# Kernel tuning notes

Hardware: AMD Instinct MI355X
Metric: run time of the kernel (lower is better)

## Reference

```python
import jax, jax.numpy as jnp
import numpy as np

B, K, L, D, H = 8, 64, 4096, 1024, 16
HD = D // H
SCALE = HD ** -0.5


def setup_inputs() -> dict:
    key = jax.random.key(0)
    ks = jax.random.split(key, 7)
    return {
        "query": jax.random.normal(ks[0], (B, K, D), jnp.float32),
        "key": jax.random.normal(ks[1], (B, L, D), jnp.float32),
        "value": jax.random.normal(ks[2], (B, L, D), jnp.float32),
        "Wq": jax.random.normal(ks[3], (D, D), jnp.float32) * (D ** -0.5),
        "Wk": jax.random.normal(ks[4], (D, D), jnp.float32) * (D ** -0.5),
        "Wv": jax.random.normal(ks[5], (D, D), jnp.float32) * (D ** -0.5),
        "Wo": jax.random.normal(ks[6], (D, D), jnp.float32) * (D ** -0.5),
        "bo": jnp.zeros((D,), jnp.float32),
    }


def reference(query, key, value, Wq, Wk, Wv, Wo, bo):
    # torch Linear: y = x @ W.T; split heads -> [B,H,len,HD]
    q = jnp.einsum('bkd,ed->bke', query, Wq).reshape(B, K, H, HD).transpose(0, 2, 1, 3)
    k = jnp.einsum('bld,ed->ble', key, Wk).reshape(B, L, H, HD).transpose(0, 2, 1, 3)
    v = jnp.einsum('bld,ed->ble', value, Wv).reshape(B, L, H, HD).transpose(0, 2, 1, 3)
    dots = jnp.einsum('bhkc,bhlc->bhkl', q, k) * SCALE  # [B,H,K,L]
    attn = jax.nn.softmax(dots, axis=-2)               # softmax over query (slot) dim
    attn = attn / (attn.sum(axis=-1, keepdims=True) + 1e-8)  # renormalize over keys
    out = jnp.einsum('bhkl,bhlc->bhkc', attn, v)       # [B,H,K,HD]
    out = out.transpose(0, 2, 1, 3).reshape(B, K, D)
    out = jnp.einsum('bkd,ed->bke', out, Wo) + bo
    return out, attn
```

## Files before the change

### kernel.cpp

```cpp
#include <hip/hip_runtime.h>
#include <hip/hip_bf16.h>

#define B_   8
#define KS_  64
#define L_   4096
#define D_   1024
#define H_   16
#define HD_  64
#define SCALE_ 0.125f

typedef __attribute__((ext_vector_type(8))) short short8;
typedef __attribute__((ext_vector_type(8))) unsigned short ushort8;
typedef __attribute__((ext_vector_type(4))) unsigned short ushort4v;
typedef __attribute__((ext_vector_type(4))) float f32x4;

__device__ __forceinline__ unsigned short f2b(float f) {
  union { float f; unsigned u; } v; v.f = f;
  unsigned r = v.u + 0x7fffu + ((v.u >> 16) & 1u);
  return (unsigned short)(r >> 16);
}

typedef const __attribute__((address_space(1))) void gas_void;
typedef __attribute__((address_space(3))) void las_void;
__device__ __forceinline__ void gl2lds16(const void* g, void* l) {
  __builtin_amdgcn_global_load_lds((gas_void*)g, (las_void*)l, 16, 0, 0);
}

__device__ __forceinline__ void bar() {
  asm volatile("" ::: "memory");
  __builtin_amdgcn_s_barrier();
  asm volatile("" ::: "memory");
}
__device__ __forceinline__ void vm4() {
  asm volatile("s_waitcnt vmcnt(4)" ::: "memory");
}

__global__ __launch_bounds__(256) void wcvt(const float* __restrict__ wq,
                                            const float* __restrict__ wk,
                                            const float* __restrict__ wv,
                                            const float* __restrict__ wo,
                                            unsigned short* __restrict__ out) {
  int i = blockIdx.x * 256 + threadIdx.x;
  int seg = i >> 18;
  int off = (i & 0x3ffff) << 2;
  const float* src = (seg == 0) ? wq : (seg == 1) ? wk : (seg == 2) ? wv : wo;
  f32x4 v = *(const f32x4*)(src + off);
  ushort4v o;
#pragma unroll
  for (int j = 0; j < 4; ++j) o[j] = f2b(v[j]);
  *(ushort4v*)(out + ((size_t)seg << 20) + off) = o;
}

__global__ __launch_bounds__(256) void cvt_qkv(const float* __restrict__ q,
                                               const float* __restrict__ k,
                                               const float* __restrict__ v,
                                               unsigned short* __restrict__ qb,
                                               unsigned short* __restrict__ kb,
                                               unsigned short* __restrict__ vb) {
  const int Q4 = 131072, K4 = 8388608;
  const int total = Q4 + 2 * K4;
  for (int i = blockIdx.x * 256 + threadIdx.x; i < total; i += gridDim.x * 256) {
    const float* src; unsigned short* dst; int off;
    if (i < Q4)            { src = q; dst = qb; off = i; }
    else if (i < Q4 + K4)  { src = k; dst = kb; off = i - Q4; }
    else                   { src = v; dst = vb; off = i - Q4 - K4; }
    f32x4 x = *(const f32x4*)(src + (size_t)off * 4);
    ushort4v o;
#pragma unroll
    for (int j = 0; j < 4; ++j) o[j] = f2b(x[j]);
    *(ushort4v*)(dst + (size_t)off * 4) = o;
  }
}

__global__ __launch_bounds__(512, 2) void gemm256(const unsigned short* __restrict__ A,
                                                  const unsigned short* __restrict__ W,
                                                  unsigned short* __restrict__ C) {
  __shared__ __align__(16) char smem[131072];
  const int tid = threadIdx.x, lane = tid & 63, w = tid >> 6;
  const int g = lane >> 4, c15 = lane & 15;
  const int wm = w >> 2, wn = w & 3;

  const int swz = (blockIdx.x & 7) * 64 + (blockIdx.x >> 3);
  const long m0 = (long)(swz >> 2) * 256;
  const int  n0 = (swz & 2 * 2 - 1) * 256;

  const int srow = w * 16 + (lane >> 2);
  const int cswz = (lane & 3) ^ ((lane >> 2) & 3);
  const unsigned short* a_sr = A + (m0 + srow) * 1024 + cswz * 8;
  const unsigned short* b_sr = W + (long)(n0 + srow) * 1024 + cswz * 8;
  const int rswz = (g ^ (c15 & 3)) << 4;
  const int aoff = (wm * 128 + c15) * 64 + rswz;
  const int boff = 65536 + (wn * 64 + c15) * 64 + rswz;

  f32x4 acc[8][4] = {};
  short8 af[8], bf[2];

  auto STAGE_A = [&](int d, int kh, int tk) {
    char* dst = smem + d * 32768 + kh * 16384 + w * 1024;
    const unsigned short* src = a_sr + tk * 64 + kh * 32;
    gl2lds16(src,          dst);
    gl2lds16(src + 131072, dst + 8192);
  };
  auto STAGE_B = [&](int d, int kh, int tk) {
    char* dst = smem + 65536 + d * 32768 + kh * 16384 + w * 1024;
    const unsigned short* src = b_sr + tk * 64 + kh * 32;
    gl2lds16(src,          dst);
    gl2lds16(src + 131072, dst + 8192);
  };
  auto LDA = [&](int d, int ks) {
    const char* base = smem + d * 32768 + ks * 16384 + aoff;
#pragma unroll
    for (int m = 0; m < 8; ++m) af[m] = *(const short8*)(base + m * 1024);
  };
  auto LDB = [&](int d, int ks, int nh) {
    const char* base = smem + d * 32768 + ks * 16384 + boff + nh * 2048;
    bf[0] = *(const short8*)(base);
    bf[1] = *(const short8*)(base + 1024);
  };
  auto MM = [&](int nh) {
    __builtin_amdgcn_s_setprio(1);
#pragma unroll
    for (int n2 = 0; n2 < 2; ++n2)
#pragma unroll
      for (int m = 0; m < 8; ++m)
        acc[m][nh * 2 + n2] =
            __builtin_amdgcn_mfma_f32_16x16x32_bf16(af[m], bf[n2], acc[m][nh * 2 + n2], 0, 0, 0);
    __builtin_amdgcn_s_setprio(0);
  };

  STAGE_A(0, 0, 0); STAGE_B(0, 0, 0); STAGE_A(0, 1, 0); STAGE_B(0, 1, 0);
  vm4();
  bar();

#pragma unroll 1
  for (int tk = 0; tk < 16; tk += 2) {
    const bool more = (tk + 2 < 16);
    LDA(0, 0); LDB(0, 0, 0); STAGE_A(1, 0, tk + 1);          bar(); MM(0); bar();
    LDB(0, 0, 1);            STAGE_B(1, 0, tk + 1);  vm4();  bar(); MM(1); bar();
    LDA(0, 1); LDB(0, 1, 0); STAGE_A(1, 1, tk + 1);          bar(); MM(0); bar();
    LDB(0, 1, 1);            STAGE_B(1, 1, tk + 1);  vm4();  bar(); MM(1); bar();
    LDA(1, 0); LDB(1, 0, 0); if (more) STAGE_A(0, 0, tk + 2);        bar(); MM(0); bar();
    LDB(1, 0, 1);            if (more) STAGE_B(0, 0, tk + 2); vm4(); bar(); MM(1); bar();
    LDA(1, 1); LDB(1, 1, 0); if (more) STAGE_A(0, 1, tk + 2);        bar(); MM(0); bar();
    LDB(1, 1, 1);            if (more) STAGE_B(0, 1, tk + 2); vm4(); bar(); MM(1); bar();
  }

  unsigned short* cl = (unsigned short*)smem;
#pragma unroll
  for (int m = 0; m < 8; ++m)
#pragma unroll
    for (int n = 0; n < 4; ++n)
#pragma unroll
      for (int r = 0; r < 4; ++r)
        cl[(wm * 128 + m * 16 + g * 4 + r) * 256 + wn * 64 + n * 16 + c15] =
            f2b(acc[m][n][r]);
  __syncthreads();
  const int row = tid >> 1, half = tid & 1;
  unsigned short*       dst = C + (m0 + row) * 1024 + n0 + half * 128;
  const unsigned short* sl  = cl + row * 256 + half * 128;
#pragma unroll
  for (int i = 0; i < 16; ++i)
    *(ushort8*)(dst + i * 8) = *(const ushort8*)(sl + i * 8);
}

template <bool OUT_F32B>
__global__ __launch_bounds__(256) void gemm_bf16(const unsigned short* __restrict__ A,
                                                 const unsigned short* __restrict__ W,
                                                 void* __restrict__ Cp,
                                                 const float* __restrict__ bias) {
  __shared__ __align__(16) char smem[34816];
  const int tid = threadIdx.x, lane = tid & 63, wv = tid >> 6;
  const int g = lane >> 4, c15 = lane & 15;
  const int wm = wv >> 1, wn = wv & 1;

  const int nwg = gridDim.x;
  const int swz = (blockIdx.x & 7) * (nwg >> 3) + (blockIdx.x >> 3);
  const long m0 = (long)(swz >> 3) * 128;
  const int  n0 = (swz & 7) * 128;

  const int srow = lane >> 2, scol = (lane & 3) * 8;
  const unsigned short* a_src = A + (m0 + srow) * 1024 + scol;
  const unsigned short* b_src = W + (long)(n0 + srow) * 1024 + scol;

  f32x4 acc[4][4] = {};

  auto stage = [&](int buf, int kt) {
    unsigned short* al = (unsigned short*)(smem + buf * 8192);
    unsigned short* bl = (unsigned short*)(smem + 16384 + buf * 8192);
#pragma unroll
    for (int q = 0; q < 2; ++q) {
      const int rbase = q * 64 + wv * 16;
      gl2lds16(a_src + (long)rbase * 1024 + kt * 32, al + rbase * 32);
      gl2lds16(b_src + (long)rbase * 1024 + kt * 32, bl + rbase * 32);
    }
  };

  stage(0, 0);
  __syncthreads();

  int cur = 0;
  for (int kt = 0; kt < 32; ++kt) {
    if (kt + 1 < 32) stage(cur ^ 1, kt + 1);
    const unsigned short* al = (const unsigned short*)(smem + cur * 8192);
    const unsigned short* bl = (const unsigned short*)(smem + 16384 + cur * 8192);
    short8 af[4];
#pragma unroll
    for (int m = 0; m < 4; ++m)
      af[m] = *(const short8*)&al[(wm * 64 + m * 16 + c15) * 32 + g * 8];
#pragma unroll
    for (int n = 0; n < 4; ++n) {
      short8 b8 = *(const short8*)&bl[(wn * 64 + n * 16 + c15) * 32 + g * 8];
#pragma unroll
      for (int m = 0; m < 4; ++m)
        acc[m][n] = __builtin_amdgcn_mfma_f32_16x16x32_bf16(af[m], b8, acc[m][n], 0, 0, 0);
    }
    __syncthreads();
    cur ^= 1;
  }

  if constexpr (OUT_F32B) {
    float* Cf = (float*)Cp;
#pragma unroll
    for (int m = 0; m < 4; ++m)
#pragma unroll
      for (int n = 0; n < 4; ++n)
#pragma unroll
        for (int r = 0; r < 4; ++r) {
          long row = m0 + wm * 64 + m * 16 + g * 4 + r;
          int  col = n0 + wn * 64 + n * 16 + c15;
          Cf[row * 1024 + col] = acc[m][n][r] + bias[col];
        }
  } else {
    unsigned short* c_lds = (unsigned short*)smem;
#pragma unroll
    for (int m = 0; m < 4; ++m)
#pragma unroll
      for (int n = 0; n < 4; ++n)
#pragma unroll
        for (int r = 0; r < 4; ++r)
          c_lds[(wm * 64 + m * 16 + g * 4 + r) * 132 + wn * 64 + n * 16 + c15] =
              f2b(acc[m][n][r]);
    __syncthreads();
    unsigned short* Cb = (unsigned short*)Cp;
    const int row = tid >> 1, half = tid & 1;
    unsigned short*       dst = Cb + (m0 + row) * 1024 + n0 + half * 64;
    const unsigned short* sl  = &c_lds[row * 132 + half * 64];
#pragma unroll
    for (int i = 0; i < 8; ++i)
      *(ushort8*)(dst + i * 8) = *(const ushort8*)(sl + i * 8);
  }
}

__global__ __launch_bounds__(512) void attn_pass1(const unsigned short* __restrict__ q_b,
                                                  const unsigned short* __restrict__ k_b,
                                                  float* __restrict__ rs_part) {
  __shared__ unsigned short q_lds[64][72];
  __shared__ unsigned short k_lds[128][72];
  __shared__ float rs_lds[8][64];
  const int bh = blockIdx.x >> 2, ch = blockIdx.x & 3;
  const int b = bh >> 4, h = bh & 15;
  const int tid = threadIdx.x;
  const int w = tid >> 6, lane = tid & 63;
  const int g = lane >> 4, c15 = lane & 15;

  {
    int slot = tid >> 3, cc = (tid & 7) * 8;
    *(ushort8*)&q_lds[slot][cc] =
        *(const ushort8*)(q_b + (long)(b * 64 + slot) * 1024 + h * 64 + cc);
  }

  float rs[4][4] = {};
  const long kbase = (long)b * L_ * D_ + h * 64;
  const int  sl = tid >> 2, sc = (tid & 3) * 16;

  for (int it = ch * 8; it < ch * 8 + 8; ++it) {
    const int l0 = it * 128;
    ushort8 k0 = *(const ushort8*)(k_b + kbase + (long)(l0 + sl) * 1024 + sc);
    ushort8 k1 = *(const ushort8*)(k_b + kbase + (long)(l0 + sl) * 1024 + sc + 8);
    __syncthreads();
    *(ushort8*)&k_lds[sl][sc]     = k0;
    *(ushort8*)&k_lds[sl][sc + 8] = k1;
    __syncthreads();

    f32x4 s[4] = {};
#pragma unroll
    for (int ks = 0; ks < 2; ++ks) {
      short8 bf = *(const short8*)&k_lds[w * 16 + c15][ks * 32 + g * 8];
#pragma unroll
      for (int m = 0; m < 4; ++m) {
        short8 af = *(const short8*)&q_lds[m * 16 + c15][ks * 32 + g * 8];
        s[m] = __builtin_amdgcn_mfma_f32_16x16x32_bf16(af, bf, s[m], 0, 0, 0);
      }
    }
    float mx = -1e30f;
#pragma unroll
    for (int m = 0; m < 4; ++m)
#pragma unroll
      for (int r = 0; r < 4; ++r) mx = fmaxf(mx, s[m][r]);
    mx = fmaxf(mx, __shfl_xor(mx, 16));
    mx = fmaxf(mx, __shfl_xor(mx, 32));
    float sum = 0.f, p[4][4];
#pragma unroll
    for (int m = 0; m < 4; ++m)
#pragma unroll
      for (int r = 0; r < 4; ++r) { p[m][r] = __expf((s[m][r] - mx) * SCALE_); sum += p[m][r]; }
    sum += __shfl_xor(sum, 16);
    sum += __shfl_xor(sum, 32);
    float rinv = 1.0f / sum;
#pragma unroll
    for (int m = 0; m < 4; ++m)
#pragma unroll
      for (int r = 0; r < 4; ++r) rs[m][r] += p[m][r] * rinv;
  }
#pragma unroll
  for (int m = 0; m < 4; ++m)
#pragma unroll
    for (int r = 0; r < 4; ++r) {
      float v = rs[m][r];
      v += __shfl_xor(v, 1); v += __shfl_xor(v, 2);
      v += __shfl_xor(v, 4); v += __shfl_xor(v, 8);
      if (c15 == 0) rs_lds[w][m * 16 + g * 4 + r] = v;
    }
  __syncthreads();
  if (tid < 64) {
    float t = 0.f;
#pragma unroll
    for (int w2 = 0; w2 < 8; ++w2) t += rs_lds[w2][tid];
    rs_part[(bh * 4 + ch) * 64 + tid] = t;
  }
}

__global__ __launch_bounds__(512) void attn_pass2(const unsigned short* __restrict__ q_b,
                                                  const unsigned short* __restrict__ k_b,
                                                  const unsigned short* __restrict__ v_b,
                                                  const float* __restrict__ rs_part,
                                                  float* __restrict__ attn,
                                                  float* __restrict__ op_part) {
  __shared__ unsigned short q_lds[64][72];
  __shared__ unsigned short k_lds[128][72];
  __shared__ unsigned short vt_lds[64][136];
  __shared__ unsigned short pt_lds[64][136];
  const int bh = blockIdx.x >> 2, ch = blockIdx.x & 3;
  const int b = bh >> 4, h = bh & 15;
  const int tid = threadIdx.x;
  const int w = tid >> 6, lane = tid & 63;
  const int g = lane >> 4, c15 = lane & 15;

  {
    int slot = tid >> 3, cc = (tid & 7) * 8;
    *(ushort8*)&q_lds[slot][cc] =
        *(const ushort8*)(q_b + (long)(b * 64 + slot) * 1024 + h * 64 + cc);
  }

  float inv_r[4][4];
#pragma unroll
  for (int m = 0; m < 4; ++m)
#pragma unroll
    for (int r = 0; r < 4; ++r) {
      int slot = m * 16 + g * 4 + r;
      float s = 0.f;
#pragma unroll
      for (int c = 0; c < 4; ++c) s += rs_part[(bh * 4 + c) * 64 + slot];
      inv_r[m][r] = 1.0f / (s + 1e-8f);
    }

  f32x4 oacc[2] = {};
  const int m_pv = w >> 1, n_pv0 = (w & 1) * 2;
  float* attn_base = attn + (long)bh * KS_ * L_;
  const long base_bld = (long)b * L_ * D_ + h * 64;
  const int  sl = tid >> 2, sc = (tid & 3) * 16;

  for (int it = ch * 8; it < ch * 8 + 8; ++it) {
    const int l0 = it * 128;
    ushort8 k0 = *(const ushort8*)(k_b + base_bld + (long)(l0 + sl) * 1024 + sc);
    ushort8 k1 = *(const ushort8*)(k_b + base_bld + (long)(l0 + sl) * 1024 + sc + 8);
    ushort8 v0 = *(const ushort8*)(v_b + base_bld + (long)(l0 + sl) * 1024 + sc);
    ushort8 v1 = *(const ushort8*)(v_b + base_bld + (long)(l0 + sl) * 1024 + sc + 8);
    __syncthreads();
    *(ushort8*)&k_lds[sl][sc]     = k0;
    *(ushort8*)&k_lds[sl][sc + 8] = k1;
#pragma unroll
    for (int j = 0; j < 8; ++j) {
      vt_lds[sc + j][sl]     = v0[j];
      vt_lds[sc + 8 + j][sl] = v1[j];
    }
    __syncthreads();

    f32x4 s[4] = {};
#pragma unroll
    for (int ks = 0; ks < 2; ++ks) {
      short8 bf = *(const short8*)&k_lds[w * 16 + c15][ks * 32 + g * 8];
#pragma unroll
      for (int m = 0; m < 4; ++m) {
        short8 af = *(const short8*)&q_lds[m * 16 + c15][ks * 32 + g * 8];
        s[m] = __builtin_amdgcn_mfma_f32_16x16x32_bf16(af, bf, s[m], 0, 0, 0);
      }
    }
    float mx = -1e30f;
#pragma unroll
    for (int m = 0; m < 4; ++m)
#pragma unroll
      for (int r = 0; r < 4; ++r) mx = fmaxf(mx, s[m][r]);
    mx = fmaxf(mx, __shfl_xor(mx, 16));
    mx = fmaxf(mx, __shfl_xor(mx, 32));
    float sum = 0.f, p[4][4];
#pragma unroll
    for (int m = 0; m < 4; ++m)
#pragma unroll
      for (int r = 0; r < 4; ++r) { p[m][r] = __expf((s[m][r] - mx) * SCALE_); sum += p[m][r]; }
    sum += __shfl_xor(sum, 16);
    sum += __shfl_xor(sum, 32);
    float rinv = 1.0f / sum;

    const int lloc = w * 16 + c15;
#pragma unroll
    for (int m = 0; m < 4; ++m)
#pragma unroll
      for (int r = 0; r < 4; ++r) {
        float ps = p[m][r] * rinv * inv_r[m][r];
        attn_base[(long)(m * 16 + g * 4 + r) * L_ + l0 + lloc] = ps;
        pt_lds[m * 16 + g * 4 + r][lloc] = f2b(ps);
      }
    __syncthreads();

#pragma unroll
    for (int ks = 0; ks < 4; ++ks) {
      short8 pa = *(const short8*)&pt_lds[m_pv * 16 + c15][ks * 32 + g * 8];
#pragma unroll
      for (int n2 = 0; n2 < 2; ++n2) {
        short8 vb = *(const short8*)&vt_lds[(n_pv0 + n2) * 16 + c15][ks * 32 + g * 8];
        oacc[n2] = __builtin_amdgcn_mfma_f32_16x16x32_bf16(pa, vb, oacc[n2], 0, 0, 0);
      }
    }
  }

#pragma unroll
  for (int n2 = 0; n2 < 2; ++n2)
#pragma unroll
    for (int r = 0; r < 4; ++r) {
      int slot = m_pv * 16 + g * 4 + r;
      int c    = (n_pv0 + n2) * 16 + c15;
      op_part[((long)(bh * 4 + ch) * 64 + slot) * 64 + c] = oacc[n2][r];
    }
}

__global__ __launch_bounds__(256) void oh_red(const float* __restrict__ op_part,
                                              unsigned short* __restrict__ oh) {
  int i = blockIdx.x * 256 + threadIdx.x;
  int c = i & 63, slot = (i >> 6) & 63, bh = i >> 12;
  float s = 0.f;
#pragma unroll
  for (int ch = 0; ch < 4; ++ch)
    s += op_part[((long)(bh * 4 + ch) * 64 + slot) * 64 + c];
  int b = bh >> 4, h = bh & 15;
  oh[(long)(b * 64 + slot) * 1024 + h * 64 + c] = f2b(s);
}

extern "C" void kernel_launch(void* const* d_in, const int* in_sizes, int n_in,
                              void* d_out, int out_size, void* d_ws, size_t ws_size,
                              hipStream_t stream) {
  (void)in_sizes; (void)n_in; (void)out_size; (void)ws_size;
  const float* query = (const float*)d_in[0];
  const float* key   = (const float*)d_in[1];
  const float* value = (const float*)d_in[2];
  const float* Wq    = (const float*)d_in[3];
  const float* Wk    = (const float*)d_in[4];
  const float* Wv    = (const float*)d_in[5];
  const float* Wo    = (const float*)d_in[6];
  const float* bo    = (const float*)d_in[7];

  char* ws = (char*)d_ws;
  unsigned short* w_all   = (unsigned short*)ws;
  unsigned short* wq_b    = w_all;
  unsigned short* wk_b    = w_all + (1u << 20);
  unsigned short* wv_b    = w_all + (2u << 20);
  unsigned short* wo_b    = w_all + (3u << 20);
  unsigned short* qin_b   = (unsigned short*)(ws + ((size_t)8  << 20));
  unsigned short* q_b     = (unsigned short*)(ws + ((size_t)9  << 20));
  unsigned short* oh_b    = (unsigned short*)(ws + ((size_t)10 << 20));
  float*          rs_part = (float*)         (ws + ((size_t)11 << 20));
  float*          op_part = (float*)         (ws + ((size_t)12 << 20));
  unsigned short* k_b     = (unsigned short*)(ws + ((size_t)20 << 20));
  unsigned short* v_b     = (unsigned short*)(ws + ((size_t)84 << 20));

  float* out  = (float*)d_out;
  float* attn = out + (size_t)B_ * KS_ * D_;

  unsigned short* kin_b = (unsigned short*)attn;
  unsigned short* vin_b = (unsigned short*)attn + ((size_t)32 << 20);

  wcvt<<<4096, 256, 0, stream>>>(Wq, Wk, Wv, Wo, w_all);
  cvt_qkv<<<2048, 256, 0, stream>>>(query, key, value, qin_b, kin_b, vin_b);

  gemm_bf16<false><<<32, 256, 0, stream>>>(qin_b, wq_b, q_b, nullptr);
  gemm256<<<512, 512, 0, stream>>>(kin_b, wk_b, k_b);
  gemm256<<<512, 512, 0, stream>>>(vin_b, wv_b, v_b);

  attn_pass1<<<512, 512, 0, stream>>>(q_b, k_b, rs_part);
  attn_pass2<<<512, 512, 0, stream>>>(q_b, k_b, v_b, rs_part, attn, op_part);
  oh_red<<<2048, 256, 0, stream>>>(op_part, oh_b);

  gemm_bf16<true><<<32, 256, 0, stream>>>(oh_b, wo_b, out, bo);
}
```

Baseline: 391.5 us.

## Fuse fp32-to-bf16 conversion of key/value into the K/V projection GEMM

Drops the separate cvt_qkv pass over key and value. The K/V projection GEMM now loads fp32 activations into registers, converts them with packed bf16 conversion instructions and writes them to LDS, while weights still stream through direct global-to-LDS loads. The query conversion is folded into the weight-conversion kernel. This removes a full read and write of the converted activations. In exchange the GEMM reads twice as many A bytes, uses more registers and needs a restructured pipeline with manual waitcnt handling.

```diff
diff --git a/kernel.cpp b/kernel.cpp
--- a/kernel.cpp
+++ b/kernel.cpp
@@ -20,6 +20,12 @@
   return (unsigned short)(r >> 16);
 }
 
+__device__ __forceinline__ unsigned cvtpk(float a, float b) {
+  unsigned r;
+  asm("v_cvt_pk_bf16_f32 %0, %1, %2" : "=v"(r) : "v"(a), "v"(b));
+  return r;
+}
+
 typedef const __attribute__((address_space(1))) void gas_void;
 typedef __attribute__((address_space(3))) void las_void;
 __device__ __forceinline__ void gl2lds16(const void* g, void* l) {
@@ -31,50 +37,42 @@
   __builtin_amdgcn_s_barrier();
   asm volatile("" ::: "memory");
 }
-__device__ __forceinline__ void vm4() {
-  asm volatile("s_waitcnt vmcnt(4)" ::: "memory");
-}
+__device__ __forceinline__ void vm0()  { asm volatile("s_waitcnt vmcnt(0)"  ::: "memory"); }
+__device__ __forceinline__ void vm2()  { asm volatile("s_waitcnt vmcnt(2)"  ::: "memory"); }
+__device__ __forceinline__ void vm10() { asm volatile("s_waitcnt vmcnt(10)" ::: "memory"); }
+__device__ __forceinline__ void lgkm0(){ asm volatile("s_waitcnt lgkmcnt(0)" ::: "memory"); }
 
 __global__ __launch_bounds__(256) void wcvt(const float* __restrict__ wq,
                                             const float* __restrict__ wk,
                                             const float* __restrict__ wv,
                                             const float* __restrict__ wo,
-                                            unsigned short* __restrict__ out) {
+                                            const float* __restrict__ query,
+                                            unsigned short* __restrict__ wout,
+                                            unsigned short* __restrict__ qout) {
   int i = blockIdx.x * 256 + threadIdx.x;
-  int seg = i >> 18;
-  int off = (i & 0x3ffff) << 2;
-  const float* src = (seg == 0) ? wq : (seg == 1) ? wk : (seg == 2) ? wv : wo;
+  const float* src;
+  unsigned short* dst;
+  int off;
+  if (i < (4 << 18)) {
+    int seg = i >> 18;
+    off = (i & 0x3ffff) << 2;
+    src = (seg == 0) ? wq : (seg == 1) ? wk : (seg == 2) ? wv : wo;
+    dst = wout + ((size_t)seg << 20);
+  } else {
+    off = (i - (4 << 18)) << 2;
+    src = query;
+    dst = qout;
+  }
   f32x4 v = *(const f32x4*)(src + off);
   ushort4v o;
 #pragma unroll
   for (int j = 0; j < 4; ++j) o[j] = f2b(v[j]);
-  *(ushort4v*)(out + ((size_t)seg << 20) + off) = o;
-}
-
-__global__ __launch_bounds__(256) void cvt_qkv(const float* __restrict__ q,
-                                               const float* __restrict__ k,
-                                               const float* __restrict__ v,
-                                               unsigned short* __restrict__ qb,
-                                               unsigned short* __restrict__ kb,
-                                               unsigned short* __restrict__ vb) {
-  const int Q4 = 131072, K4 = 8388608;
-  const int total = Q4 + 2 * K4;
-  for (int i = blockIdx.x * 256 + threadIdx.x; i < total; i += gridDim.x * 256) {
-    const float* src; unsigned short* dst; int off;
-    if (i < Q4)            { src = q; dst = qb; off = i; }
-    else if (i < Q4 + K4)  { src = k; dst = kb; off = i - Q4; }
-    else                   { src = v; dst = vb; off = i - Q4 - K4; }
-    f32x4 x = *(const f32x4*)(src + (size_t)off * 4);
-    ushort4v o;
-#pragma unroll
-    for (int j = 0; j < 4; ++j) o[j] = f2b(x[j]);
-    *(ushort4v*)(dst + (size_t)off * 4) = o;
-  }
-}
-
-__global__ __launch_bounds__(512, 2) void gemm256(const unsigned short* __restrict__ A,
-                                                  const unsigned short* __restrict__ W,
-                                                  unsigned short* __restrict__ C) {
+  *(ushort4v*)(dst + off) = o;
+}
+
+__global__ __launch_bounds__(512, 2) void gemm256f(const float* __restrict__ A,
+                                                   const unsigned short* __restrict__ W,
+                                                   unsigned short* __restrict__ C) {
   __shared__ __align__(16) char smem[131072];
   const int tid = threadIdx.x, lane = tid & 63, w = tid >> 6;
   const int g = lane >> 4, c15 = lane & 15;
@@ -82,31 +80,56 @@
 
   const int swz = (blockIdx.x & 7) * 64 + (blockIdx.x >> 3);
   const long m0 = (long)(swz >> 2) * 256;
-  const int  n0 = (swz & 2 * 2 - 1) * 256;
+  const int  n0 = (swz & 3) * 256;
 
   const int srow = w * 16 + (lane >> 2);
   const int cswz = (lane & 3) ^ ((lane >> 2) & 3);
-  const unsigned short* a_sr = A + (m0 + srow) * 1024 + cswz * 8;
   const unsigned short* b_sr = W + (long)(n0 + srow) * 1024 + cswz * 8;
+  const float* a32 = A + (m0 + srow) * 1024 + (lane & 3) * 8;
+  const int    c0  = ((lane & 3) ^ ((lane >> 2) & 3)) << 4;
+
   const int rswz = (g ^ (c15 & 3)) << 4;
   const int aoff = (wm * 128 + c15) * 64 + rswz;
   const int boff = 65536 + (wn * 64 + c15) * 64 + rswz;
 
   f32x4 acc[8][4] = {};
   short8 af[8], bf[2];
-
-  auto STAGE_A = [&](int d, int kh, int tk) {
-    char* dst = smem + d * 32768 + kh * 16384 + w * 1024;
-    const unsigned short* src = a_sr + tk * 64 + kh * 32;
-    gl2lds16(src,          dst);
-    gl2lds16(src + 131072, dst + 8192);
-  };
+  f32x4 av[8];
+
   auto STAGE_B = [&](int d, int kh, int tk) {
     char* dst = smem + 65536 + d * 32768 + kh * 16384 + w * 1024;
     const unsigned short* src = b_sr + tk * 64 + kh * 32;
     gl2lds16(src,          dst);
     gl2lds16(src + 131072, dst + 8192);
   };
+  auto ISSUE_A = [&](int tk) {
+    const float* p = a32 + tk * 64;
+    av[0] = *(const f32x4*)(p);
+    av[1] = *(const f32x4*)(p + 4);
+    av[2] = *(const f32x4*)(p + 131072);
+    av[3] = *(const f32x4*)(p + 131072 + 4);
+    av[4] = *(const f32x4*)(p + 32);
+    av[5] = *(const f32x4*)(p + 36);
+    av[6] = *(const f32x4*)(p + 131072 + 32);
+    av[7] = *(const f32x4*)(p + 131072 + 36);
+  };
+  auto CVTWRITE_A = [&](int d) {
+    char* b0 = smem + d * 32768;
+    char* b1 = b0 + 16384;
+    union { unsigned u[4]; ushort8 s; } t0, t1, t2, t3;
+    t0.u[0] = cvtpk(av[0][0], av[0][1]); t0.u[1] = cvtpk(av[0][2], av[0][3]);
+    t0.u[2] = cvtpk(av[1][0], av[1][1]); t0.u[3] = cvtpk(av[1][2], av[1][3]);
+    t1.u[0] = cvtpk(av[2][0], av[2][1]); t1.u[1] = cvtpk(av[2][2], av[2][3]);
+    t1.u[2] = cvtpk(av[3][0], av[3][1]); t1.u[3] = cvtpk(av[3][2], av[3][3]);
+    t2.u[0] = cvtpk(av[4][0], av[4][1]); t2.u[1] = cvtpk(av[4][2], av[4][3]);
+    t2.u[2] = cvtpk(av[5][0], av[5][1]); t2.u[3] = cvtpk(av[5][2], av[5][3]);
+    t3.u[0] = cvtpk(av[6][0], av[6][1]); t3.u[1] = cvtpk(av[6][2], av[6][3]);
+    t3.u[2] = cvtpk(av[7][0], av[7][1]); t3.u[3] = cvtpk(av[7][2], av[7][3]);
+    *(ushort8*)(b0 + srow * 64 + c0)        = t0.s;
+    *(ushort8*)(b0 + srow * 64 + 8192 + c0) = t1.s;
+    *(ushort8*)(b1 + srow * 64 + c0)        = t2.s;
+    *(ushort8*)(b1 + srow * 64 + 8192 + c0) = t3.s;
+  };
   auto LDA = [&](int d, int ks) {
     const char* base = smem + d * 32768 + ks * 16384 + aoff;
 #pragma unroll
@@ -128,22 +151,43 @@
     __builtin_amdgcn_s_setprio(0);
   };
 
-  STAGE_A(0, 0, 0); STAGE_B(0, 0, 0); STAGE_A(0, 1, 0); STAGE_B(0, 1, 0);
-  vm4();
+  auto GROUP = [&](int d, int tk, bool stage, bool issue2, bool last) {
+    LDA(d, 0); LDB(d, 0, 0);
+    bar(); MM(0); bar();
+    LDB(d, 0, 1);
+    if (stage) STAGE_B(d ^ 1, 0, tk + 1);
+    if (last) vm0(); else vm10();
+    bar(); MM(1); bar();
+    LDA(d, 1); LDB(d, 1, 0);
+    bar(); MM(0); bar();
+    LDB(d, 1, 1);
+    if (stage) {
+      STAGE_B(d ^ 1, 1, tk + 1);
+      vm2();
+      CVTWRITE_A(d ^ 1);
+      if (issue2) ISSUE_A(tk + 2);
+      lgkm0();
+    }
+    bar(); MM(1); bar();
+  };
+
+  ISSUE_A(0);
+  STAGE_B(0, 0, 0);
+  vm2();
+  CVTWRITE_A(0);
+  STAGE_B(0, 1, 0);
+  ISSUE_A(1);
+  vm10();
+  lgkm0();
   bar();
 
 #pragma unroll 1
-  for (int tk = 0; tk < 16; tk += 2) {
-    const bool more = (tk + 2 < 16);
-    LDA(0, 0); LDB(0, 0, 0); STAGE_A(1, 0, tk + 1);          bar(); MM(0); bar();
-    LDB(0, 0, 1);            STAGE_B(1, 0, tk + 1);  vm4();  bar(); MM(1); bar();
-    LDA(0, 1); LDB(0, 1, 0); STAGE_A(1, 1, tk + 1);          bar(); MM(0); bar();
-    LDB(0, 1, 1);            STAGE_B(1, 1, tk + 1);  vm4();  bar(); MM(1); bar();
-    LDA(1, 0); LDB(1, 0, 0); if (more) STAGE_A(0, 0, tk + 2);        bar(); MM(0); bar();
-    LDB(1, 0, 1);            if (more) STAGE_B(0, 0, tk + 2); vm4(); bar(); MM(1); bar();
-    LDA(1, 1); LDB(1, 1, 0); if (more) STAGE_A(0, 1, tk + 2);        bar(); MM(0); bar();
-    LDB(1, 1, 1);            if (more) STAGE_B(0, 1, tk + 2); vm4(); bar(); MM(1); bar();
-  }
+  for (int tk = 0; tk < 14; tk += 2) {
+    GROUP(0, tk,     true, true,  false);
+    GROUP(1, tk + 1, true, true,  false);
+  }
+  GROUP(0, 14, true,  false, false);
+  GROUP(1, 15, false, false, true);
 
   unsigned short* cl = (unsigned short*)smem;
 #pragma unroll
@@ -486,15 +530,11 @@
   float* out  = (float*)d_out;
   float* attn = out + (size_t)B_ * KS_ * D_;
 
-  unsigned short* kin_b = (unsigned short*)attn;
-  unsigned short* vin_b = (unsigned short*)attn + ((size_t)32 << 20);
-
-  wcvt<<<4096, 256, 0, stream>>>(Wq, Wk, Wv, Wo, w_all);
-  cvt_qkv<<<2048, 256, 0, stream>>>(query, key, value, qin_b, kin_b, vin_b);
+  wcvt<<<4608, 256, 0, stream>>>(Wq, Wk, Wv, Wo, query, w_all, qin_b);
 
   gemm_bf16<false><<<32, 256, 0, stream>>>(qin_b, wq_b, q_b, nullptr);
-  gemm256<<<512, 512, 0, stream>>>(kin_b, wk_b, k_b);
-  gemm256<<<512, 512, 0, stream>>>(vin_b, wv_b, v_b);
+  gemm256f<<<512, 512, 0, stream>>>(key,   wk_b, k_b);
+  gemm256f<<<512, 512, 0, stream>>>(value, wv_b, v_b);
 
   attn_pass1<<<512, 512, 0, stream>>>(q_b, k_b, rs_part);
   attn_pass2<<<512, 512, 0, stream>>>(q_b, k_b, v_b, rs_part, attn, op_part);
```

Result: slower. 578.2 us (+47.7%).
